# Kernel optimization log

Hardware: AMD Instinct MI355X
Metric: run time of the kernel (lower is better)

The kernel has to match this reference:

```python
import jax, jax.numpy as jnp
import numpy as np

M = 100_000   # output rows of neighborhood matrix
N = 100_000   # nodes
D = 64        # feature dim (in_channels)
OUT = 64      # out_channels
NNZ = 1_600_000
NEG_SLOPE = 0.2


def setup_inputs() -> dict:
    key = jax.random.key(0)
    k1, k2, k3, k4, k5 = jax.random.split(key, 5)
    # ensure every row has at least one neighbor (torch min init is +inf otherwise)
    rows = jnp.concatenate([jnp.arange(M, dtype=jnp.int32),
                            jax.random.randint(k1, (NNZ - M,), 0, M, dtype=jnp.int32)])
    cols = jax.random.randint(k2, (NNZ,), 0, N, dtype=jnp.int32)
    vals = jnp.ones((NNZ,), jnp.float32)
    node_features = jax.random.normal(k3, (N, D), jnp.float32)
    W = jax.random.normal(k4, (OUT, 12 * D), jnp.float32) / jnp.sqrt(12.0 * D)
    b = jax.random.normal(k5, (OUT,), jnp.float32) * 0.01
    return {"rows": rows, "cols": cols, "vals": vals,
            "node_features": node_features, "W": W, "b": b}


def reference(rows, cols, vals, node_features, W, b):
    gathered = node_features[cols]                      # [nnz, D]
    deg = jax.ops.segment_sum(vals, rows, num_segments=M)[:, None]  # [M,1]
    valid = deg > 0
    safe_deg = jnp.where(valid, deg, 1.0)

    # mean = spmm(A, X) / deg on valid rows (torch leaves invalid rows as raw sum = 0)
    sums = jax.ops.segment_sum(vals[:, None] * gathered, rows, num_segments=M)
    mean = jnp.where(valid, sums / safe_deg, sums)

    # torch max starts from zeros -> clamps at 0 from below; empty rows stay 0
    maxf = jnp.zeros((M, D), node_features.dtype).at[rows].max(gathered)
    # torch min starts from +inf; all rows covered by construction
    minf = jnp.full((M, D), jnp.inf, node_features.dtype).at[rows].min(gathered)

    sq = jax.ops.segment_sum(vals[:, None] * gathered**2, rows, num_segments=M)
    sq = jnp.where(valid, sq / safe_deg, sq)
    std = jnp.sqrt(jnp.clip(sq - mean**2, 0.0))

    logd = jnp.log10(deg + 2.0)                          # [M,1]
    delta = jnp.mean(logd)
    s = logd / delta

    # per aggregator: identity, amplification (*s), attenuation (/s)
    feats = [t for a in (mean, maxf, minf, std) for t in (a, a * s, a / s)]
    X = jnp.concatenate(feats, axis=1)                   # [M, 12*D]
    out = X @ W.T + b
    return jnp.where(out >= 0, out, NEG_SLOPE * out)
```

## Files before the change

### kernel.cpp

```cpp
#include <hip/hip_runtime.h>
#include <cstdint>

#define M_ROWS   100000
#define N_NODES  100000
#define NNZ_E    1600000
#define K_DIM    768
#define NCHUNK   24
#define NEG_SLOPE 0.2f
#define NBUK     391
#define BCAP     5120
#define EPB      4096

using f32x4 = __attribute__((ext_vector_type(4))) float;
using f16x8 = __attribute__((ext_vector_type(8))) _Float16;
using f16x4 = __attribute__((ext_vector_type(4))) _Float16;

#define OFF_CNT    0u
#define OFF_RS     401408u
#define OFF_PART   802816u
#define OFF_DELTA  804864u
#define OFF_GCUR   805120u
#define OFF_BINCSR 807168u
#define OFF_WB     8814848u
#define OFF_NFH    8913152u
#define WS_NEEDED  21713152u

__global__ void k_wb(const float* __restrict__ W, _Float16* __restrict__ Wb) {
  int idx = blockIdx.x * blockDim.x + threadIdx.x;
  if (idx < NCHUNK * 4 * 64 * 8) {
    int i  = idx & 7;
    int l  = (idx >> 3) & 63;
    int n  = (idx >> 9) & 3;
    int kc = idx >> 11;
    int k  = kc * 32 + ((l >> 4) << 3) + i;
    int o  = n * 16 + (l & 15);
    Wb[idx] = (_Float16)W[o * K_DIM + k];
  }
}

__global__ void k_nf(const float* __restrict__ nf, _Float16* __restrict__ nfh,
                     int* __restrict__ gcur) {
  const int gid = blockIdx.x * 256 + threadIdx.x;
  if (gid < NBUK) gcur[gid] = gid * BCAP;
  const int i = gid * 4;
  if (i < N_NODES * 64) {
    const f32x4 v = *reinterpret_cast<const f32x4*>(nf + i);
    f16x4 h;
    #pragma unroll
    for (int j = 0; j < 4; ++j) h[j] = (_Float16)v[j];
    *reinterpret_cast<f16x4*>(nfh + i) = h;
  }
}

__global__ void k_seed(int* __restrict__ gcur) {
  int b = blockIdx.x * blockDim.x + threadIdx.x;
  if (b < NBUK) gcur[b] = b * BCAP;
}

__global__ __launch_bounds__(256) void k_bin(const int* __restrict__ rows,
                                             const int* __restrict__ cols,
                                             int* __restrict__ gcur,
                                             int* __restrict__ binArr) {
  __shared__ int hist[NBUK];
  __shared__ int base_s[NBUK];
  const int t  = threadIdx.x;
  const int e0 = blockIdx.x * EPB;
  for (int b = t; b < NBUK; b += 256) hist[b] = 0;
  __syncthreads();
  #pragma unroll
  for (int i = 0; i < EPB / 256; ++i) {
    const int e = e0 + i * 256 + t;
    if (e < NNZ_E) atomicAdd(&hist[rows[e] >> 8], 1);
  }
  __syncthreads();
  for (int b = t; b < NBUK; b += 256) {
    const int h = hist[b];
    base_s[b] = h ? atomicAdd(&gcur[b], h) : 0;
    hist[b] = 0;
  }
  __syncthreads();
  #pragma unroll
  for (int i = 0; i < EPB / 256; ++i) {
    const int e = e0 + i * 256 + t;
    if (e < NNZ_E) {
      const int r = rows[e], c = cols[e], b = r >> 8;
      const int p = atomicAdd(&hist[b], 1);
      const int slot = base_s[b] + p;
      if (slot < (b + 1) * BCAP)
        binArr[slot] = ((r & 255) << 24) | c;
    }
  }
}

__global__ __launch_bounds__(256) void k_sortbucket(int* __restrict__ bincsr,
                                                    const int* __restrict__ gcur,
                                                    int* __restrict__ cnt,
                                                    int* __restrict__ row_start,
                                                    float* __restrict__ partial) {
  __shared__ int se[BCAP];
  __shared__ int hist[256];
  __shared__ int curs[256];
  __shared__ int sd[256];
  __shared__ float wsum[4];
  const int b = blockIdx.x, t = threadIdx.x;
  const int s0  = b * BCAP;
  const int len = min(gcur[b] - s0, BCAP);
  for (int i = t; i < len; i += 256) se[i] = bincsr[s0 + i];
  hist[t] = 0;
  __syncthreads();
  for (int i = t; i < len; i += 256)
    atomicAdd(&hist[((unsigned)se[i]) >> 24], 1);
  __syncthreads();
  const int h = hist[t];
  const int r = (b << 8) + t;
  sd[t] = h;
  __syncthreads();
  #pragma unroll
  for (int off = 1; off < 256; off <<= 1) {
    int add = (t >= off) ? sd[t - off] : 0;
    __syncthreads();
    sd[t] += add;
    __syncthreads();
  }
  const int excl = sd[t] - h;
  curs[t] = excl;
  if (r < M_ROWS) {
    cnt[r] = h;
    row_start[r] = s0 + excl;
  }
  float ls = (r < M_ROWS) ? log10f((float)h + 2.0f) : 0.f;
  #pragma unroll
  for (int off = 32; off > 0; off >>= 1) ls += __shfl_xor(ls, off);
  if ((t & 63) == 0) wsum[t >> 6] = ls;
  __syncthreads();
  if (t == 0) partial[b] = wsum[0] + wsum[1] + wsum[2] + wsum[3];
  for (int i = t; i < len; i += 256) {
    const int e  = se[i];
    const int rl = (int)(((unsigned)e) >> 24);
    const int p  = atomicAdd(&curs[rl], 1);
    bincsr[s0 + p] = (e & 0x00FFFFFF) << 7;
  }
}

__global__ void k_delta(const float* __restrict__ partial, float* __restrict__ delta) {
  __shared__ float sd[256];
  const int t = threadIdx.x;
  float s = 0.f;
  for (int i = t; i < NBUK; i += 256) s += partial[i];
  sd[t] = s;
  __syncthreads();
  for (int off = 128; off > 0; off >>= 1) {
    if (t < off) sd[t] += sd[t + off];
    __syncthreads();
  }
  if (t == 0) delta[0] = sd[0] / (float)M_ROWS;
}

template <bool F16NF>
__global__ __launch_bounds__(256) void k_main(
    const float* __restrict__ nf32, const _Float16* __restrict__ nfh,
    const int* __restrict__ csr, const int* __restrict__ rs,
    const int* __restrict__ cnt, const float* __restrict__ delta_p,
    const _Float16* __restrict__ Wb, const float* __restrict__ bias,
    float* __restrict__ out)
{
  __shared__ _Float16 xs[32][264];
  __shared__ float s_s[32];

  const int tid  = threadIdx.x;
  const int w    = tid >> 6;
  const int lane = tid & 63;
  const int g    = lane >> 4;
  const int q    = lane & 15;
  const int r0   = blockIdx.x * 32;
  const float delta = delta_p[0];

  const char* nfb = (const char*)nfh + q * 8;

  #pragma unroll
  for (int pass = 0; pass < 2; ++pass) {
    const int rl = w * 8 + pass * 4 + g;
    const int r  = r0 + rl;
    const int js = rs[r];
    const int len = cnt[r];
    const int je1 = js + len - 1;
    int ml = len;
    ml = max(ml, __shfl_xor(ml, 16));
    ml = max(ml, __shfl_xor(ml, 32));

    f16x4 hsum = {}; f16x4 hsq = {}; f16x4 hmx = {};
    f16x4 hmn = {(_Float16)INFINITY, (_Float16)INFINITY,
                 (_Float16)INFINITY, (_Float16)INFINITY};

    auto ldx = [&](int off) -> f16x4 {
      if constexpr (F16NF) {
        return *reinterpret_cast<const f16x4*>(nfb + off);
      } else {
        const f32x4 v = *reinterpret_cast<const f32x4*>(
            (const char*)nf32 + (size_t)off * 2 + q * 16);
        f16x4 h;
        #pragma unroll
        for (int j2 = 0; j2 < 4; ++j2) h[j2] = (_Float16)v[j2];
        return h;
      }
    };

    int o0 = csr[min(js + 0, je1)];
    int o1 = csr[min(js + 1, je1)];
    int o2 = csr[min(js + 2, je1)];
    int o3 = csr[min(js + 3, je1)];
    int o4 = csr[min(js + 4, je1)];
    int o5 = csr[min(js + 5, je1)];
    int o6 = csr[min(js + 6, je1)];
    int o7 = csr[min(js + 7, je1)];

    for (int t = 0; t < ml; t += 8) {
      const int p0 = o0, p1 = o1, p2 = o2, p3 = o3;
      const int p4 = o4, p5 = o5, p6 = o6, p7 = o7;
      const int tn = t + 8;
      if (tn < ml) {
        o0 = csr[min(js + tn + 0, je1)];
        o1 = csr[min(js + tn + 1, je1)];
        o2 = csr[min(js + tn + 2, je1)];
        o3 = csr[min(js + tn + 3, je1)];
        o4 = csr[min(js + tn + 4, je1)];
        o5 = csr[min(js + tn + 5, je1)];
        o6 = csr[min(js + tn + 6, je1)];
        o7 = csr[min(js + tn + 7, je1)];
      }
      const f16x4 x0 = ldx(p0), x1 = ldx(p1), x2 = ldx(p2), x3 = ldx(p3);
      const f16x4 x4 = ldx(p4), x5 = ldx(p5), x6 = ldx(p6), x7 = ldx(p7);
      const f16x4 z = {};
      const f16x4 m0 = (t + 0 < len) ? x0 : z;
      const f16x4 m1 = (t + 1 < len) ? x1 : z;
      const f16x4 m2 = (t + 2 < len) ? x2 : z;
      const f16x4 m3 = (t + 3 < len) ? x3 : z;
      const f16x4 m4 = (t + 4 < len) ? x4 : z;
      const f16x4 m5 = (t + 5 < len) ? x5 : z;
      const f16x4 m6 = (t + 6 < len) ? x6 : z;
      const f16x4 m7 = (t + 7 < len) ? x7 : z;
      hmx = __builtin_elementwise_max(hmx, x0); hmn = __builtin_elementwise_min(hmn, x0);
      hsum += m0; hsq += m0 * x0;
      hmx = __builtin_elementwise_max(hmx, x1); hmn = __builtin_elementwise_min(hmn, x1);
      hsum += m1; hsq += m1 * x1;
      hmx = __builtin_elementwise_max(hmx, x2); hmn = __builtin_elementwise_min(hmn, x2);
      hsum += m2; hsq += m2 * x2;
      hmx = __builtin_elementwise_max(hmx, x3); hmn = __builtin_elementwise_min(hmn, x3);
      hsum += m3; hsq += m3 * x3;
      hmx = __builtin_elementwise_max(hmx, x4); hmn = __builtin_elementwise_min(hmn, x4);
      hsum += m4; hsq += m4 * x4;
      hmx = __builtin_elementwise_max(hmx, x5); hmn = __builtin_elementwise_min(hmn, x5);
      hsum += m5; hsq += m5 * x5;
      hmx = __builtin_elementwise_max(hmx, x6); hmn = __builtin_elementwise_min(hmn, x6);
      hsum += m6; hsq += m6 * x6;
      hmx = __builtin_elementwise_max(hmx, x7); hmn = __builtin_elementwise_min(hmn, x7);
      hsum += m7; hsq += m7 * x7;
    }

    const float dg   = (float)len;
    const float safe = (dg > 0.f) ? dg : 1.0f;
    const float inv  = 1.0f / safe;
    f16x4 hmean, hstd;
    #pragma unroll
    for (int i = 0; i < 4; ++i) {
      const float mean = (float)hsum[i] * inv;
      const float sqm  = (float)hsq[i] * inv;
      const float var  = fmaxf(sqm - mean * mean, 0.f);
      hmean[i] = (_Float16)mean;
      hstd[i]  = (_Float16)sqrtf(var);
    }
    *reinterpret_cast<f16x4*>(&xs[rl][0 * 64 + q * 4]) = hmean;
    *reinterpret_cast<f16x4*>(&xs[rl][1 * 64 + q * 4]) = hmx;
    *reinterpret_cast<f16x4*>(&xs[rl][2 * 64 + q * 4]) = hmn;
    *reinterpret_cast<f16x4*>(&xs[rl][3 * 64 + q * 4]) = hstd;
    if (q == 0) s_s[rl] = log10f(dg + 2.0f) / delta;
  }
  __syncthreads();

  f32x4 acc0 = {0.f, 0.f, 0.f, 0.f}, acc1 = {0.f, 0.f, 0.f, 0.f};
  const int khi = lane >> 4;
  const float sA = s_s[q];
  const float sB = s_s[16 + q];
  const f16x8 sA8  = (f16x8)(_Float16)sA;
  const f16x8 isA8 = (f16x8)(_Float16)(1.0f / sA);
  const f16x8 sB8  = (f16x8)(_Float16)sB;
  const f16x8 isB8 = (f16x8)(_Float16)(1.0f / sB);

  #pragma unroll
  for (int kc = 0; kc < NCHUNK; ++kc) {
    const int kb = kc >> 1;
    const int a  = kb / 3;
    const int tt = kb - 3 * a;
    const int off = a * 64 + ((kc & 1) << 5) + (khi << 3);
    f16x8 a0 = *reinterpret_cast<const f16x8*>(&xs[q][off]);
    f16x8 a1 = *reinterpret_cast<const f16x8*>(&xs[16 + q][off]);
    if (tt == 1) { a0 = a0 * sA8;  a1 = a1 * sB8; }
    if (tt == 2) { a0 = a0 * isA8; a1 = a1 * isB8; }
    const f16x8 bf = *reinterpret_cast<const f16x8*>(Wb + ((size_t)(kc * 4 + w) * 64 + lane) * 8);
    acc0 = __builtin_amdgcn_mfma_f32_16x16x32_f16(a0, bf, acc0, 0, 0, 0);
    acc1 = __builtin_amdgcn_mfma_f32_16x16x32_f16(a1, bf, acc1, 0, 0, 0);
  }

  const int col = w * 16 + q;
  const float bv = bias[col];
  #pragma unroll
  for (int i = 0; i < 4; ++i) {
    const int rr = khi * 4 + i;
    float v = acc0[i] + bv;
    v = (v >= 0.f) ? v : NEG_SLOPE * v;
    out[(size_t)(r0 + rr) * 64 + col] = v;
    float u = acc1[i] + bv;
    u = (u >= 0.f) ? u : NEG_SLOPE * u;
    out[(size_t)(r0 + 16 + rr) * 64 + col] = u;
  }
}

extern "C" void kernel_launch(void* const* d_in, const int* in_sizes, int n_in,
                              void* d_out, int out_size, void* d_ws, size_t ws_size,
                              hipStream_t stream) {
  const int*   rows = (const int*)d_in[0];
  const int*   cols = (const int*)d_in[1];
  const float* nf   = (const float*)d_in[3];
  const float* W    = (const float*)d_in[4];
  const float* bias = (const float*)d_in[5];
  float* out = (float*)d_out;

  char* ws = (char*)d_ws;
  int*      cnt       = (int*)(ws + OFF_CNT);
  int*      row_start = (int*)(ws + OFF_RS);
  float*    partial   = (float*)(ws + OFF_PART);
  float*    delta     = (float*)(ws + OFF_DELTA);
  int*      gcur      = (int*)(ws + OFF_GCUR);
  int*      bincsr    = (int*)(ws + OFF_BINCSR);
  _Float16* Wb        = (_Float16*)(ws + OFF_WB);
  _Float16* nfh       = (_Float16*)(ws + OFF_NFH);

  const bool f16path = (ws_size >= WS_NEEDED);

  k_wb<<<192, 256, 0, stream>>>(W, Wb);
  if (f16path) k_nf<<<6250, 256, 0, stream>>>(nf, nfh, gcur);
  else         k_seed<<<2, 256, 0, stream>>>(gcur);
  k_bin<<<(NNZ_E + EPB - 1) / EPB, 256, 0, stream>>>(rows, cols, gcur, bincsr);
  k_sortbucket<<<NBUK, 256, 0, stream>>>(bincsr, gcur, cnt, row_start, partial);
  k_delta<<<1, 256, 0, stream>>>(partial, delta);
  if (f16path)
    k_main<true><<<3125, 256, 0, stream>>>(nf, nfh, bincsr, row_start, cnt, delta, Wb, bias, out);
  else
    k_main<false><<<3125, 256, 0, stream>>>(nf, nfh, bincsr, row_start, cnt, delta, Wb, bias, out);
}
```

Baseline: 103.5 us.

## Split neighbor gather across two half-groups with 16-byte loads and shuffle reduction

Each 16-lane row group now splits into two halves that walk alternating neighbors. Each lane loads 16 bytes (8 halfs) per neighbor instead of 8, and the halves merge sum, sq, max and min with xor-8 shuffles. The main loop covers full chunks of 8 neighbors without masking or prefetch, and a separate masked tail handles the rest. This aims to raise bytes per load and remove per-iteration masking, at the cost of dropping the index prefetch and adding shuffle work.

```diff
diff --git a/kernel.cpp b/kernel.cpp
--- a/kernel.cpp
+++ b/kernel.cpp
@@ -172,108 +172,128 @@
   const int lane = tid & 63;
   const int g    = lane >> 4;
   const int q    = lane & 15;
+  const int h    = (lane >> 3) & 1;
+  const int d    = lane & 7;
   const int r0   = blockIdx.x * 32;
   const float delta = delta_p[0];
-
-  const char* nfb = (const char*)nfh + q * 8;
+  const int d16  = d * 16;
+
+  auto ld16 = [&](int off) -> f16x8 {
+    if constexpr (F16NF) {
+      return *reinterpret_cast<const f16x8*>((const char*)nfh + off + d16);
+    } else {
+      const char* p = (const char*)nf32 + (size_t)off * 2 + d * 32;
+      const f32x4 a = *reinterpret_cast<const f32x4*>(p);
+      const f32x4 c = *reinterpret_cast<const f32x4*>(p + 16);
+      f16x8 x;
+      #pragma unroll
+      for (int j = 0; j < 4; ++j) { x[j] = (_Float16)a[j]; x[4 + j] = (_Float16)c[j]; }
+      return x;
+    }
+  };
+
+  auto xor8 = [&](f16x8 v) -> f16x8 {
+    union { f16x8 hh; int ii[4]; } u;
+    u.hh = v;
+    #pragma unroll
+    for (int k = 0; k < 4; ++k) u.ii[k] = __shfl_xor(u.ii[k], 8);
+    return u.hh;
+  };
 
   #pragma unroll
   for (int pass = 0; pass < 2; ++pass) {
-    const int rl = w * 8 + pass * 4 + g;
-    const int r  = r0 + rl;
-    const int js = rs[r];
+    const int rl  = w * 8 + pass * 4 + g;
+    const int r   = r0 + rl;
+    const int js  = rs[r];
     const int len = cnt[r];
-    const int je1 = js + len - 1;
-    int ml = len;
-    ml = max(ml, __shfl_xor(ml, 16));
-    ml = max(ml, __shfl_xor(ml, 32));
-
-    f16x4 hsum = {}; f16x4 hsq = {}; f16x4 hmx = {};
-    f16x4 hmn = {(_Float16)INFINITY, (_Float16)INFINITY,
+    const int full8 = len & ~7;
+    const int tailn = len - full8;
+    int mfull = full8, mtail = tailn;
+    mfull = max(mfull, __shfl_xor(mfull, 16));
+    mfull = max(mfull, __shfl_xor(mfull, 32));
+    mtail = max(mtail, __shfl_xor(mtail, 16));
+    mtail = max(mtail, __shfl_xor(mtail, 32));
+
+    f16x8 hsum = {}; f16x8 hsq = {}; f16x8 hmx = {};
+    f16x8 hmn = {(_Float16)INFINITY, (_Float16)INFINITY, (_Float16)INFINITY,
+                 (_Float16)INFINITY, (_Float16)INFINITY, (_Float16)INFINITY,
                  (_Float16)INFINITY, (_Float16)INFINITY};
 
-    auto ldx = [&](int off) -> f16x4 {
-      if constexpr (F16NF) {
-        return *reinterpret_cast<const f16x4*>(nfb + off);
-      } else {
-        const f32x4 v = *reinterpret_cast<const f32x4*>(
-            (const char*)nf32 + (size_t)off * 2 + q * 16);
-        f16x4 h;
-        #pragma unroll
-        for (int j2 = 0; j2 < 4; ++j2) h[j2] = (_Float16)v[j2];
-        return h;
+    const int jb = js + h;
+
+    for (int t = 0; t < mfull; t += 8) {
+      if (t < full8) {
+        const int i0 = csr[jb + t + 0];
+        const int i1 = csr[jb + t + 2];
+        const int i2 = csr[jb + t + 4];
+        const int i3 = csr[jb + t + 6];
+        const f16x8 x0 = ld16(i0), x1 = ld16(i1), x2 = ld16(i2), x3 = ld16(i3);
+        hmx = __builtin_elementwise_max(hmx, x0);
+        hmn = __builtin_elementwise_min(hmn, x0);
+        hsum += x0; hsq += x0 * x0;
+        hmx = __builtin_elementwise_max(hmx, x1);
+        hmn = __builtin_elementwise_min(hmn, x1);
+        hsum += x1; hsq += x1 * x1;
+        hmx = __builtin_elementwise_max(hmx, x2);
+        hmn = __builtin_elementwise_min(hmn, x2);
+        hsum += x2; hsq += x2 * x2;
+        hmx = __builtin_elementwise_max(hmx, x3);
+        hmn = __builtin_elementwise_min(hmn, x3);
+        hsum += x3; hsq += x3 * x3;
       }
-    };
-
-    int o0 = csr[min(js + 0, je1)];
-    int o1 = csr[min(js + 1, je1)];
-    int o2 = csr[min(js + 2, je1)];
-    int o3 = csr[min(js + 3, je1)];
-    int o4 = csr[min(js + 4, je1)];
-    int o5 = csr[min(js + 5, je1)];
-    int o6 = csr[min(js + 6, je1)];
-    int o7 = csr[min(js + 7, je1)];
-
-    for (int t = 0; t < ml; t += 8) {
-      const int p0 = o0, p1 = o1, p2 = o2, p3 = o3;
-      const int p4 = o4, p5 = o5, p6 = o6, p7 = o7;
-      const int tn = t + 8;
-      if (tn < ml) {
-        o0 = csr[min(js + tn + 0, je1)];
-        o1 = csr[min(js + tn + 1, je1)];
-        o2 = csr[min(js + tn + 2, je1)];
-        o3 = csr[min(js + tn + 3, je1)];
-        o4 = csr[min(js + tn + 4, je1)];
-        o5 = csr[min(js + tn + 5, je1)];
-        o6 = csr[min(js + tn + 6, je1)];
-        o7 = csr[min(js + tn + 7, je1)];
-      }
-      const f16x4 x0 = ldx(p0), x1 = ldx(p1), x2 = ldx(p2), x3 = ldx(p3);
-      const f16x4 x4 = ldx(p4), x5 = ldx(p5), x6 = ldx(p6), x7 = ldx(p7);
-      const f16x4 z = {};
-      const f16x4 m0 = (t + 0 < len) ? x0 : z;
-      const f16x4 m1 = (t + 1 < len) ? x1 : z;
-      const f16x4 m2 = (t + 2 < len) ? x2 : z;
-      const f16x4 m3 = (t + 3 < len) ? x3 : z;
-      const f16x4 m4 = (t + 4 < len) ? x4 : z;
-      const f16x4 m5 = (t + 5 < len) ? x5 : z;
-      const f16x4 m6 = (t + 6 < len) ? x6 : z;
-      const f16x4 m7 = (t + 7 < len) ? x7 : z;
-      hmx = __builtin_elementwise_max(hmx, x0); hmn = __builtin_elementwise_min(hmn, x0);
+    }
+
+    if (mtail > 0) {
+      const int last = js + len - 1;
+      const int e0 = full8 + 0 + h, e1 = full8 + 2 + h;
+      const int e2 = full8 + 4 + h, e3 = full8 + 6 + h;
+      const int i0 = csr[min(jb + full8 + 0, last)];
+      const int i1 = csr[min(jb + full8 + 2, last)];
+      const int i2 = csr[min(jb + full8 + 4, last)];
+      const int i3 = csr[min(jb + full8 + 6, last)];
+      const f16x8 x0 = ld16(i0), x1 = ld16(i1), x2 = ld16(i2), x3 = ld16(i3);
+      const f16x8 z = {};
+      const f16x8 m0 = (e0 < len) ? x0 : z;
+      const f16x8 m1 = (e1 < len) ? x1 : z;
+      const f16x8 m2 = (e2 < len) ? x2 : z;
+      const f16x8 m3 = (e3 < len) ? x3 : z;
+      hmx = __builtin_elementwise_max(hmx, x0);
+      hmn = __builtin_elementwise_min(hmn, x0);
       hsum += m0; hsq += m0 * x0;
-      hmx = __builtin_elementwise_max(hmx, x1); hmn = __builtin_elementwise_min(hmn, x1);
+      hmx = __builtin_elementwise_max(hmx, x1);
+      hmn = __builtin_elementwise_min(hmn, x1);
       hsum += m1; hsq += m1 * x1;
-      hmx = __builtin_elementwise_max(hmx, x2); hmn = __builtin_elementwise_min(hmn, x2);
+      hmx = __builtin_elementwise_max(hmx, x2);
+      hmn = __builtin_elementwise_min(hmn, x2);
       hsum += m2; hsq += m2 * x2;
-      hmx = __builtin_elementwise_max(hmx, x3); hmn = __builtin_elementwise_min(hmn, x3);
+      hmx = __builtin_elementwise_max(hmx, x3);
+      hmn = __builtin_elementwise_min(hmn, x3);
       hsum += m3; hsq += m3 * x3;
-      hmx = __builtin_elementwise_max(hmx, x4); hmn = __builtin_elementwise_min(hmn, x4);
-      hsum += m4; hsq += m4 * x4;
-      hmx = __builtin_elementwise_max(hmx, x5); hmn = __builtin_elementwise_min(hmn, x5);
-      hsum += m5; hsq += m5 * x5;
-      hmx = __builtin_elementwise_max(hmx, x6); hmn = __builtin_elementwise_min(hmn, x6);
-      hsum += m6; hsq += m6 * x6;
-      hmx = __builtin_elementwise_max(hmx, x7); hmn = __builtin_elementwise_min(hmn, x7);
-      hsum += m7; hsq += m7 * x7;
-    }
-
-    const float dg   = (float)len;
-    const float safe = (dg > 0.f) ? dg : 1.0f;
-    const float inv  = 1.0f / safe;
-    f16x4 hmean, hstd;
+    }
+
+    hsum += xor8(hsum);
+    hsq  += xor8(hsq);
+    hmx = __builtin_elementwise_max(hmx, xor8(hmx));
+    hmn = __builtin_elementwise_min(hmn, xor8(hmn));
+
+    const float dg  = (float)len;
+    const float inv = 1.0f / fmaxf(dg, 1.0f);
+    f16x8 hmean, hstd;
     #pragma unroll
-    for (int i = 0; i < 4; ++i) {
+    for (int i = 0; i < 8; ++i) {
       const float mean = (float)hsum[i] * inv;
       const float sqm  = (float)hsq[i] * inv;
       const float var  = fmaxf(sqm - mean * mean, 0.f);
       hmean[i] = (_Float16)mean;
       hstd[i]  = (_Float16)sqrtf(var);
     }
-    *reinterpret_cast<f16x4*>(&xs[rl][0 * 64 + q * 4]) = hmean;
-    *reinterpret_cast<f16x4*>(&xs[rl][1 * 64 + q * 4]) = hmx;
-    *reinterpret_cast<f16x4*>(&xs[rl][2 * 64 + q * 4]) = hmn;
-    *reinterpret_cast<f16x4*>(&xs[rl][3 * 64 + q * 4]) = hstd;
-    if (q == 0) s_s[rl] = log10f(dg + 2.0f) / delta;
+    if (h == 0) {
+      *reinterpret_cast<f16x8*>(&xs[rl][0 * 64 + d * 8]) = hmean;
+      *reinterpret_cast<f16x8*>(&xs[rl][1 * 64 + d * 8]) = hmx;
+      *reinterpret_cast<f16x8*>(&xs[rl][2 * 64 + d * 8]) = hmn;
+      *reinterpret_cast<f16x8*>(&xs[rl][3 * 64 + d * 8]) = hstd;
+      if (q == 0) s_s[rl] = log10f(dg + 2.0f) / delta;
+    }
   }
   __syncthreads();
 
```

Result: no change. 103.6 us (+0.1%).
